# Performance work log

Measured on AMD Instinct MI355X. Metric: run time of the kernel, lower is better.

Reference implementation:

```python
import jax, jax.numpy as jnp
import numpy as np

NUM_HEADS = 4
EMBED_DIM = 256
HEAD_DIM = EMBED_DIM // NUM_HEADS
B, N = 4, 4096


def setup_inputs() -> dict:
    key = jax.random.key(0)
    kq, kk, kv, kw = jax.random.split(key, 4)
    q = jax.random.normal(kq, (B, N, EMBED_DIM), dtype=jnp.float32)
    k = jax.random.normal(kk, (B, N, EMBED_DIM), dtype=jnp.float32)
    v = jax.random.normal(kv, (B, N, EMBED_DIM), dtype=jnp.float32)
    W_out = jax.random.normal(kw, (EMBED_DIM, EMBED_DIM), dtype=jnp.float32) * (1.0 / np.sqrt(EMBED_DIM))
    b_out = jnp.zeros((EMBED_DIM,), dtype=jnp.float32)
    return {"q": q, "k": k, "v": v, "W_out": W_out, "b_out": b_out}


def reference(q, k, v, W_out, b_out):
    b, n, _ = q.shape
    # [b, n, e] -> [b, h, n, d]
    qh = q.reshape(b, n, NUM_HEADS, HEAD_DIM).transpose(0, 2, 1, 3)
    kh = k.reshape(b, n, NUM_HEADS, HEAD_DIM).transpose(0, 2, 1, 3)
    vh = v.reshape(b, n, NUM_HEADS, HEAD_DIM).transpose(0, 2, 1, 3)
    scale = 1.0 / jnp.sqrt(jnp.asarray(HEAD_DIM, dtype=qh.dtype))
    # full [b, h, n, n] score matrix, as in the original module
    attn = jnp.einsum('bhqd,bhkd->bhqk', qh, kh) * scale
    attn = jax.nn.softmax(attn, axis=-1)
    out = jnp.einsum('bhqk,bhkd->bhqd', attn, vh)
    out = out.transpose(0, 2, 1, 3).reshape(b, n, EMBED_DIM)
    # nn.Linear: x @ W.T + b
    return out @ W_out.T + b_out
```

## Files before the change

kernel.cpp:

```cpp
#include <hip/hip_runtime.h>
#include <hip/hip_bf16.h>

#define B_ 4
#define H_ 4
#define N_ 4096
#define D_ 64
#define E_ 256
#define KVB 64
#define QBLK 128
#define NT (N_ / KVB)

typedef short short8 __attribute__((ext_vector_type(8)));
typedef float f32x4 __attribute__((ext_vector_type(4)));
typedef float f32x16 __attribute__((ext_vector_type(16)));

__device__ __forceinline__ ushort f2bf(float f) {
  union { float f; unsigned u; } a; a.f = f;
  unsigned r = a.u + 0x7fffu + ((a.u >> 16) & 1u);
  return (ushort)(r >> 16);
}

__device__ __forceinline__ uint4 pack8(float a0, float a1, float a2, float a3,
                                       float a4, float a5, float a6, float a7) {
  uint4 u;
  u.x = (unsigned)f2bf(a0) | ((unsigned)f2bf(a1) << 16);
  u.y = (unsigned)f2bf(a2) | ((unsigned)f2bf(a3) << 16);
  u.z = (unsigned)f2bf(a4) | ((unsigned)f2bf(a5) << 16);
  u.w = (unsigned)f2bf(a6) | ((unsigned)f2bf(a7) << 16);
  return u;
}

__device__ __forceinline__ unsigned cvt_pk_bf16(float lo, float hi) {
  unsigned r;
  asm("v_cvt_pk_bf16_f32 %0, %1, %2" : "=v"(r) : "v"(lo), "v"(hi));
  return r;
}

__device__ __forceinline__ void permlane32_swap(unsigned &a, unsigned &b) {
  asm volatile("v_permlane32_swap_b32 %0, %1" : "+v"(a), "+v"(b));
}

__global__ void cast_w_kernel(const float* __restrict__ W, ushort* __restrict__ Wb) {
  int i = blockIdx.x * blockDim.x + threadIdx.x;
  float4 x = ((const float4*)W)[i];
  ushort4 o;
  o.x = f2bf(x.x); o.y = f2bf(x.y); o.z = f2bf(x.z); o.w = f2bf(x.w);
  ((ushort4*)Wb)[i] = o;
}

__global__ void prep_kv(const float* __restrict__ k, const float* __restrict__ v,
                        ushort* __restrict__ Kb, ushort* __restrict__ Vtb) {
  __shared__ float kt[64][65];
  __shared__ float vt[64][65];
  const int gid = blockIdx.x;
  const int bh = gid >> 6, t = gid & 63;
  const int b = bh >> 2, h = bh & 3;
  const int tid = threadIdx.x;
  const int rr = tid >> 4, cc = (tid & 15) * 4;
  const float* kg = k + ((size_t)b * N_ + t * 64) * E_ + h * 64;
  const float* vg = v + ((size_t)b * N_ + t * 64) * E_ + h * 64;
  ushort* ko = Kb + (size_t)gid * 4096;
  ushort* vo = Vtb + (size_t)gid * 4096;

  for (int it = 0; it < 4; ++it) {
    int r = rr + it * 16;
    float4 kx = *(const float4*)(kg + (size_t)r * E_ + cc);
    float4 vx = *(const float4*)(vg + (size_t)r * E_ + cc);
    kt[r][cc] = kx.x; kt[r][cc + 1] = kx.y; kt[r][cc + 2] = kx.z; kt[r][cc + 3] = kx.w;
    vt[r][cc] = vx.x; vt[r][cc + 1] = vx.y; vt[r][cc + 2] = vx.z; vt[r][cc + 3] = vx.w;
  }
  __syncthreads();

  for (int j = 0; j < 2; ++j) {
    int u = j * 256 + tid;
    int frag = u >> 6, l = u & 63;
    int a = (frag >> 2) * 32 + (l & 31);
    int c0 = (frag & 3) * 16 + ((l >> 5) & 1) * 8;
    *(uint4*)(ko + u * 8) = pack8(kt[a][c0], kt[a][c0 + 1], kt[a][c0 + 2], kt[a][c0 + 3],
                                  kt[a][c0 + 4], kt[a][c0 + 5], kt[a][c0 + 6], kt[a][c0 + 7]);
    *(uint4*)(vo + u * 8) = pack8(vt[c0][a], vt[c0 + 1][a], vt[c0 + 2][a], vt[c0 + 3][a],
                                  vt[c0 + 4][a], vt[c0 + 5][a], vt[c0 + 6][a], vt[c0 + 7][a]);
  }
}

__launch_bounds__(256, 2)
__global__ void attn_kernel(const float* __restrict__ q,
                            const ushort* __restrict__ Kb,
                            const ushort* __restrict__ Vtb,
                            ushort* __restrict__ X) {
  __shared__ __attribute__((aligned(16))) ushort SM[2][2][4096];
  __shared__ float Lb[2][2][32];
  __shared__ float Lb2[2][2][32];

  const int bid = blockIdx.x;
  const int swz = (bid & 7) * 64 + (bid >> 3);
  const int bh = swz >> 5;
  const int qt = swz & 31;
  const int b = bh >> 2, h = bh & 3;
  const int tid = threadIdx.x;
  const int wid = tid >> 6;
  const int wq = wid & 1;
  const int kh = wid >> 1;
  const int lane = tid & 63;
  const int ln = lane & 31;
  const int hi = lane >> 5;

  const char* Kg = (const char*)Kb + (size_t)bh * NT * 8192;
  const char* Vg = (const char*)Vtb + (size_t)bh * NT * 8192;

  const float SC = 0.125f * 1.44269504f;
  const int qrow0 = qt * QBLK + wq * 64;
  short8 qf[2][4];
#pragma unroll
  for (int qg = 0; qg < 2; ++qg) {
    const float* Qg = q + ((size_t)b * N_ + qrow0 + qg * 32 + ln) * E_ + h * D_;
#pragma unroll
    for (int ks = 0; ks < 4; ++ks) {
      const float* p = Qg + ks * 16 + hi * 8;
      float4 x0 = *(const float4*)(p);
      float4 x1 = *(const float4*)(p + 4);
      short8 f;
      f[0] = (short)f2bf(x0.x * SC); f[1] = (short)f2bf(x0.y * SC);
      f[2] = (short)f2bf(x0.z * SC); f[3] = (short)f2bf(x0.w * SC);
      f[4] = (short)f2bf(x1.x * SC); f[5] = (short)f2bf(x1.y * SC);
      f[6] = (short)f2bf(x1.z * SC); f[7] = (short)f2bf(x1.w * SC);
      qf[qg][ks] = f;
    }
  }

  f32x16 O00 = (f32x16)0.0f, O01 = (f32x16)0.0f;
  f32x16 O10 = (f32x16)0.0f, O11 = (f32x16)0.0f;
  float lsum0 = 0.f, lsum1 = 0.f;

  {
    uint4 a0 = *(const uint4*)(Kg + tid * 16);
    uint4 a1 = *(const uint4*)(Kg + 4096 + tid * 16);
    uint4 a2 = *(const uint4*)(Vg + tid * 16);
    uint4 a3 = *(const uint4*)(Vg + 4096 + tid * 16);
    *(uint4*)((char*)&SM[0][0][0] + tid * 16) = a0;
    *(uint4*)((char*)&SM[0][0][0] + 4096 + tid * 16) = a1;
    *(uint4*)((char*)&SM[0][1][0] + tid * 16) = a2;
    *(uint4*)((char*)&SM[0][1][0] + 4096 + tid * 16) = a3;
  }
  __syncthreads();
  int cur = 0;

  for (int t = 0; t < NT; ++t) {
    const bool pfn = (t + 1 < NT);
    uint4 rk0, rk1, rv0, rv1;
    if (pfn) {
      const char* kg = Kg + (size_t)(t + 1) * 8192;
      const char* vg = Vg + (size_t)(t + 1) * 8192;
      rk0 = *(const uint4*)(kg + tid * 16);
      rk1 = *(const uint4*)(kg + 4096 + tid * 16);
      rv0 = *(const uint4*)(vg + tid * 16);
      rv1 = *(const uint4*)(vg + 4096 + tid * 16);
    }

    const char* Kl = (const char*)&SM[cur][0][0];
    const char* Vl = (const char*)&SM[cur][1][0];

    short8 kf[4];
#pragma unroll
    for (int ks = 0; ks < 4; ++ks)
      kf[ks] = *(short8*)(Kl + (kh * 4 + ks) * 1024 + lane * 16);

    f32x16 S0 = (f32x16)0.0f, S1 = (f32x16)0.0f;
    __builtin_amdgcn_s_setprio(1);
#pragma unroll
    for (int ks = 0; ks < 4; ++ks) {
      S0 = __builtin_amdgcn_mfma_f32_32x32x16_bf16(kf[ks], qf[0][ks], S0, 0, 0, 0);
      S1 = __builtin_amdgcn_mfma_f32_32x32x16_bf16(kf[ks], qf[1][ks], S1, 0, 0, 0);
    }
    __builtin_amdgcn_s_setprio(0);

    short8 vf[2][2];
#pragma unroll
    for (int db = 0; db < 2; ++db)
#pragma unroll
      for (int s = 0; s < 2; ++s)
        vf[db][s] = *(short8*)(Vl + (db * 4 + kh * 2 + s) * 1024 + lane * 16);

    float p0[16], p1[16];
#pragma unroll
    for (int i = 0; i < 16; ++i) {
      p0[i] = __builtin_amdgcn_exp2f(S0[i]);
      p1[i] = __builtin_amdgcn_exp2f(S1[i]);
    }
    {
      float s1[8];
#pragma unroll
      for (int i = 0; i < 8; ++i) s1[i] = p0[2 * i] + p0[2 * i + 1];
#pragma unroll
      for (int i = 0; i < 4; ++i) s1[i] = s1[2 * i] + s1[2 * i + 1];
      lsum0 += (s1[0] + s1[1]) + (s1[2] + s1[3]);
#pragma unroll
      for (int i = 0; i < 8; ++i) s1[i] = p1[2 * i] + p1[2 * i + 1];
#pragma unroll
      for (int i = 0; i < 4; ++i) s1[i] = s1[2 * i] + s1[2 * i + 1];
      lsum1 += (s1[0] + s1[1]) + (s1[2] + s1[3]);
    }

    short8 pa0[2], pa1[2];
#pragma unroll
    for (int s = 0; s < 2; ++s) {
      int base = s * 8;
      {
        unsigned w0 = cvt_pk_bf16(p0[base + 0], p0[base + 1]);
        unsigned w2 = cvt_pk_bf16(p0[base + 4], p0[base + 5]);
        permlane32_swap(w0, w2);
        unsigned w1 = cvt_pk_bf16(p0[base + 2], p0[base + 3]);
        unsigned w3 = cvt_pk_bf16(p0[base + 6], p0[base + 7]);
        permlane32_swap(w1, w3);
        uint4 u; u.x = w0; u.y = w1; u.z = w2; u.w = w3;
        union { uint4 u4; short8 s8; } cv; cv.u4 = u;
        pa0[s] = cv.s8;
      }
      {
        unsigned w0 = cvt_pk_bf16(p1[base + 0], p1[base + 1]);
        unsigned w2 = cvt_pk_bf16(p1[base + 4], p1[base + 5]);
        permlane32_swap(w0, w2);
        unsigned w1 = cvt_pk_bf16(p1[base + 2], p1[base + 3]);
        unsigned w3 = cvt_pk_bf16(p1[base + 6], p1[base + 7]);
        permlane32_swap(w1, w3);
        uint4 u; u.x = w0; u.y = w1; u.z = w2; u.w = w3;
        union { uint4 u4; short8 s8; } cv; cv.u4 = u;
        pa1[s] = cv.s8;
      }
    }

    if (pfn) {
      *(uint4*)((char*)&SM[cur ^ 1][0][0] + tid * 16) = rk0;
      *(uint4*)((char*)&SM[cur ^ 1][0][0] + 4096 + tid * 16) = rk1;
      *(uint4*)((char*)&SM[cur ^ 1][1][0] + tid * 16) = rv0;
      *(uint4*)((char*)&SM[cur ^ 1][1][0] + 4096 + tid * 16) = rv1;
    }

    __builtin_amdgcn_s_setprio(1);
#pragma unroll
    for (int s = 0; s < 2; ++s) {
      O00 = __builtin_amdgcn_mfma_f32_32x32x16_bf16(pa0[s], vf[0][s], O00, 0, 0, 0);
      O01 = __builtin_amdgcn_mfma_f32_32x32x16_bf16(pa0[s], vf[1][s], O01, 0, 0, 0);
      O10 = __builtin_amdgcn_mfma_f32_32x32x16_bf16(pa1[s], vf[0][s], O10, 0, 0, 0);
      O11 = __builtin_amdgcn_mfma_f32_32x32x16_bf16(pa1[s], vf[1][s], O11, 0, 0, 0);
    }
    __builtin_amdgcn_s_setprio(0);

    __syncthreads();
    cur ^= 1;
  }

  float l0 = lsum0 + __shfl_xor(lsum0, 32);
  float l1 = lsum1 + __shfl_xor(lsum1, 32);
  float* Ox = (float*)&SM[0][0][0];
  if (kh) {
    if (lane < 32) { Lb[wq][0][ln] = l0; Lb[wq][1][ln] = l1; }
#pragma unroll
    for (int r2 = 0; r2 < 16; ++r2) {
      Ox[wq * 4096 + 0 * 2048 + 0 * 1024 + r2 * 64 + lane] = O00[r2];
      Ox[wq * 4096 + 0 * 2048 + 1 * 1024 + r2 * 64 + lane] = O01[r2];
      Ox[wq * 4096 + 1 * 2048 + 0 * 1024 + r2 * 64 + lane] = O10[r2];
      Ox[wq * 4096 + 1 * 2048 + 1 * 1024 + r2 * 64 + lane] = O11[r2];
    }
  }
  __syncthreads();
  if (!kh) {
    float lt0 = l0 + Lb[wq][0][ln];
    float lt1 = l1 + Lb[wq][1][ln];
    if (lane < 32) { Lb2[wq][0][ln] = lt0; Lb2[wq][1][ln] = lt1; }
    asm volatile("" ::: "memory");
#pragma unroll
    for (int r2 = 0; r2 < 16; ++r2) {
      O00[r2] += Ox[wq * 4096 + 0 * 2048 + 0 * 1024 + r2 * 64 + lane];
      O01[r2] += Ox[wq * 4096 + 0 * 2048 + 1 * 1024 + r2 * 64 + lane];
      O10[r2] += Ox[wq * 4096 + 1 * 2048 + 0 * 1024 + r2 * 64 + lane];
      O11[r2] += Ox[wq * 4096 + 1 * 2048 + 1 * 1024 + r2 * 64 + lane];
    }
    ushort* Xp = X + ((size_t)b * N_) * E_ + h * D_;
#pragma unroll
    for (int r2 = 0; r2 < 16; ++r2) {
      int crow = (r2 & 3) + 8 * (r2 >> 2) + 4 * hi;
      float i0 = 1.0f / Lb2[wq][0][crow];
      float i1 = 1.0f / Lb2[wq][1][crow];
      int q0 = qrow0 + crow;
      int q1 = qrow0 + 32 + crow;
      Xp[(size_t)q0 * E_ + ln]      = f2bf(O00[r2] * i0);
      Xp[(size_t)q0 * E_ + 32 + ln] = f2bf(O01[r2] * i0);
      Xp[(size_t)q1 * E_ + ln]      = f2bf(O10[r2] * i1);
      Xp[(size_t)q1 * E_ + 32 + ln] = f2bf(O11[r2] * i1);
    }
  }
}

__launch_bounds__(256, 2)
__global__ void proj_kernel(const ushort* __restrict__ X, const ushort* __restrict__ Wb,
                            const float* __restrict__ bias, float* __restrict__ out) {
  const int m0   = blockIdx.x * 64;
  const int tid  = threadIdx.x;
  const int wid  = tid >> 6;
  const int lane = tid & 63;
  const int g    = lane >> 4;
  const int lr   = lane & 15;
  const int n0   = wid * 64;

  f32x4 acc[4][4];
  for (int mb = 0; mb < 4; ++mb)
    for (int nb = 0; nb < 4; ++nb)
      acc[mb][nb] = (f32x4){0.f, 0.f, 0.f, 0.f};

  for (int k0 = 0; k0 < E_; k0 += 32) {
    short8 af[4], bfr[4];
    for (int mb = 0; mb < 4; ++mb)
      af[mb] = *(const short8*)(X + (size_t)(m0 + mb * 16 + lr) * E_ + k0 + g * 8);
    for (int nb = 0; nb < 4; ++nb)
      bfr[nb] = *(const short8*)(Wb + (size_t)(n0 + nb * 16 + lr) * E_ + k0 + g * 8);
    for (int mb = 0; mb < 4; ++mb)
      for (int nb = 0; nb < 4; ++nb)
        acc[mb][nb] = __builtin_amdgcn_mfma_f32_16x16x32_bf16(af[mb], bfr[nb], acc[mb][nb], 0, 0, 0);
  }

  for (int nb = 0; nb < 4; ++nb) {
    float bv = bias[n0 + nb * 16 + lr];
    for (int mb = 0; mb < 4; ++mb)
      for (int r = 0; r < 4; ++r)
        out[(size_t)(m0 + mb * 16 + g * 4 + r) * E_ + n0 + nb * 16 + lr] = acc[mb][nb][r] + bv;
  }
}

extern "C" void kernel_launch(void* const* d_in, const int* in_sizes, int n_in,
                              void* d_out, int out_size, void* d_ws, size_t ws_size,
                              hipStream_t stream) {
  const float* q    = (const float*)d_in[0];
  const float* k    = (const float*)d_in[1];
  const float* v    = (const float*)d_in[2];
  const float* W    = (const float*)d_in[3];
  const float* bias = (const float*)d_in[4];

  char* ws = (char*)d_ws;
  ushort* X   = (ushort*)ws;
  ushort* Wb  = (ushort*)(ws + 8388608);
  ushort* Kb  = (ushort*)(ws + 8388608 + 131072);
  ushort* Vtb = (ushort*)(ws + 8388608 + 131072 + 8388608);

  cast_w_kernel<<<64, 256, 0, stream>>>(W, Wb);
  prep_kv<<<B_ * H_ * NT, 256, 0, stream>>>(k, v, Kb, Vtb);
  attn_kernel<<<B_ * H_ * (N_ / QBLK), 256, 0, stream>>>(q, Kb, Vtb, X);
  proj_kernel<<<(B_ * N_) / 64, 256, 0, stream>>>(X, Wb, bias, (float*)d_out);
}
```

Measured before the change: 108.9 us.

## Process two KV tiles per loop iteration with doubled shared-memory stages

The attention main loop now handles two 64-key tiles per iteration. The shared buffers are doubled to hold a pair of K/V tiles, and the prefetch of the next pair is issued after both QK^T MFMA groups. This halves the number of block-wide barriers and lets the second tile's score MFMAs overlap with the first tile's softmax and PV work. In exchange it doubles LDS usage to 64KB and needs more registers for the extra score accumulators and 8 prefetch registers, which may reduce occupancy under the 2-blocks-per-CU launch bound.

```diff
diff --git a/kernel.cpp b/kernel.cpp
--- a/kernel.cpp
+++ b/kernel.cpp
@@ -9,6 +9,7 @@
 #define KVB 64
 #define QBLK 128
 #define NT (N_ / KVB)
+#define NR (NT / 2)
 
 typedef short short8 __attribute__((ext_vector_type(8)));
 typedef float f32x4 __attribute__((ext_vector_type(4)));
@@ -88,7 +89,7 @@
                             const ushort* __restrict__ Kb,
                             const ushort* __restrict__ Vtb,
                             ushort* __restrict__ X) {
-  __shared__ __attribute__((aligned(16))) ushort SM[2][2][4096];
+  __shared__ __attribute__((aligned(16))) ushort SM[2][2][2][4096];
   __shared__ float Lb[2][2][32];
   __shared__ float Lb2[2][2][32];
 
@@ -133,118 +134,211 @@
   float lsum0 = 0.f, lsum1 = 0.f;
 
   {
-    uint4 a0 = *(const uint4*)(Kg + tid * 16);
-    uint4 a1 = *(const uint4*)(Kg + 4096 + tid * 16);
-    uint4 a2 = *(const uint4*)(Vg + tid * 16);
-    uint4 a3 = *(const uint4*)(Vg + 4096 + tid * 16);
-    *(uint4*)((char*)&SM[0][0][0] + tid * 16) = a0;
-    *(uint4*)((char*)&SM[0][0][0] + 4096 + tid * 16) = a1;
-    *(uint4*)((char*)&SM[0][1][0] + tid * 16) = a2;
-    *(uint4*)((char*)&SM[0][1][0] + 4096 + tid * 16) = a3;
+#pragma unroll
+    for (int c = 0; c < 2; ++c) {
+      uint4 a0 = *(const uint4*)(Kg + (size_t)c * 8192 + tid * 16);
+      uint4 a1 = *(const uint4*)(Kg + (size_t)c * 8192 + 4096 + tid * 16);
+      uint4 a2 = *(const uint4*)(Vg + (size_t)c * 8192 + tid * 16);
+      uint4 a3 = *(const uint4*)(Vg + (size_t)c * 8192 + 4096 + tid * 16);
+      *(uint4*)((char*)&SM[0][c][0][0] + tid * 16) = a0;
+      *(uint4*)((char*)&SM[0][c][0][0] + 4096 + tid * 16) = a1;
+      *(uint4*)((char*)&SM[0][c][1][0] + tid * 16) = a2;
+      *(uint4*)((char*)&SM[0][c][1][0] + 4096 + tid * 16) = a3;
+    }
   }
   __syncthreads();
   int cur = 0;
 
-  for (int t = 0; t < NT; ++t) {
-    const bool pfn = (t + 1 < NT);
-    uint4 rk0, rk1, rv0, rv1;
+  for (int r = 0; r < NR; ++r) {
+    const bool pfn = (r + 1 < NR);
+
+    const char* KlA = (const char*)&SM[cur][0][0][0];
+    const char* VlA = (const char*)&SM[cur][0][1][0];
+    const char* KlB = (const char*)&SM[cur][1][0][0];
+    const char* VlB = (const char*)&SM[cur][1][1][0];
+
+    short8 kfA[4];
+#pragma unroll
+    for (int ks = 0; ks < 4; ++ks)
+      kfA[ks] = *(short8*)(KlA + (kh * 4 + ks) * 1024 + lane * 16);
+    f32x16 SA0 = (f32x16)0.0f, SA1 = (f32x16)0.0f;
+    __builtin_amdgcn_s_setprio(1);
+#pragma unroll
+    for (int ks = 0; ks < 4; ++ks) {
+      SA0 = __builtin_amdgcn_mfma_f32_32x32x16_bf16(kfA[ks], qf[0][ks], SA0, 0, 0, 0);
+      SA1 = __builtin_amdgcn_mfma_f32_32x32x16_bf16(kfA[ks], qf[1][ks], SA1, 0, 0, 0);
+    }
+    __builtin_amdgcn_s_setprio(0);
+
+    short8 kfB[4];
+#pragma unroll
+    for (int ks = 0; ks < 4; ++ks)
+      kfB[ks] = *(short8*)(KlB + (kh * 4 + ks) * 1024 + lane * 16);
+    f32x16 SB0 = (f32x16)0.0f, SB1 = (f32x16)0.0f;
+    __builtin_amdgcn_s_setprio(1);
+#pragma unroll
+    for (int ks = 0; ks < 4; ++ks) {
+      SB0 = __builtin_amdgcn_mfma_f32_32x32x16_bf16(kfB[ks], qf[0][ks], SB0, 0, 0, 0);
+      SB1 = __builtin_amdgcn_mfma_f32_32x32x16_bf16(kfB[ks], qf[1][ks], SB1, 0, 0, 0);
+    }
+    __builtin_amdgcn_s_setprio(0);
+
+    uint4 st[8];
     if (pfn) {
-      const char* kg = Kg + (size_t)(t + 1) * 8192;
-      const char* vg = Vg + (size_t)(t + 1) * 8192;
-      rk0 = *(const uint4*)(kg + tid * 16);
-      rk1 = *(const uint4*)(kg + 4096 + tid * 16);
-      rv0 = *(const uint4*)(vg + tid * 16);
-      rv1 = *(const uint4*)(vg + 4096 + tid * 16);
-    }
-
-    const char* Kl = (const char*)&SM[cur][0][0];
-    const char* Vl = (const char*)&SM[cur][1][0];
-
-    short8 kf[4];
-#pragma unroll
-    for (int ks = 0; ks < 4; ++ks)
-      kf[ks] = *(short8*)(Kl + (kh * 4 + ks) * 1024 + lane * 16);
-
-    f32x16 S0 = (f32x16)0.0f, S1 = (f32x16)0.0f;
-    __builtin_amdgcn_s_setprio(1);
-#pragma unroll
-    for (int ks = 0; ks < 4; ++ks) {
-      S0 = __builtin_amdgcn_mfma_f32_32x32x16_bf16(kf[ks], qf[0][ks], S0, 0, 0, 0);
-      S1 = __builtin_amdgcn_mfma_f32_32x32x16_bf16(kf[ks], qf[1][ks], S1, 0, 0, 0);
-    }
-    __builtin_amdgcn_s_setprio(0);
-
-    short8 vf[2][2];
-#pragma unroll
-    for (int db = 0; db < 2; ++db)
-#pragma unroll
-      for (int s = 0; s < 2; ++s)
-        vf[db][s] = *(short8*)(Vl + (db * 4 + kh * 2 + s) * 1024 + lane * 16);
-
-    float p0[16], p1[16];
-#pragma unroll
-    for (int i = 0; i < 16; ++i) {
-      p0[i] = __builtin_amdgcn_exp2f(S0[i]);
-      p1[i] = __builtin_amdgcn_exp2f(S1[i]);
-    }
+      const char* kg = Kg + (size_t)(2 * r + 2) * 8192;
+      const char* vg = Vg + (size_t)(2 * r + 2) * 8192;
+#pragma unroll
+      for (int c = 0; c < 2; ++c) {
+        st[c * 4 + 0] = *(const uint4*)(kg + (size_t)c * 8192 + tid * 16);
+        st[c * 4 + 1] = *(const uint4*)(kg + (size_t)c * 8192 + 4096 + tid * 16);
+        st[c * 4 + 2] = *(const uint4*)(vg + (size_t)c * 8192 + tid * 16);
+        st[c * 4 + 3] = *(const uint4*)(vg + (size_t)c * 8192 + 4096 + tid * 16);
+      }
+    }
+
     {
-      float s1[8];
-#pragma unroll
-      for (int i = 0; i < 8; ++i) s1[i] = p0[2 * i] + p0[2 * i + 1];
-#pragma unroll
-      for (int i = 0; i < 4; ++i) s1[i] = s1[2 * i] + s1[2 * i + 1];
-      lsum0 += (s1[0] + s1[1]) + (s1[2] + s1[3]);
-#pragma unroll
-      for (int i = 0; i < 8; ++i) s1[i] = p1[2 * i] + p1[2 * i + 1];
-#pragma unroll
-      for (int i = 0; i < 4; ++i) s1[i] = s1[2 * i] + s1[2 * i + 1];
-      lsum1 += (s1[0] + s1[1]) + (s1[2] + s1[3]);
-    }
-
-    short8 pa0[2], pa1[2];
-#pragma unroll
-    for (int s = 0; s < 2; ++s) {
-      int base = s * 8;
+      short8 vf[2][2];
+#pragma unroll
+      for (int db = 0; db < 2; ++db)
+#pragma unroll
+        for (int s = 0; s < 2; ++s)
+          vf[db][s] = *(short8*)(VlA + (db * 4 + kh * 2 + s) * 1024 + lane * 16);
+
+      float p0[16], p1[16];
+#pragma unroll
+      for (int i = 0; i < 16; ++i) {
+        p0[i] = __builtin_amdgcn_exp2f(SA0[i]);
+        p1[i] = __builtin_amdgcn_exp2f(SA1[i]);
+      }
       {
-        unsigned w0 = cvt_pk_bf16(p0[base + 0], p0[base + 1]);
-        unsigned w2 = cvt_pk_bf16(p0[base + 4], p0[base + 5]);
-        permlane32_swap(w0, w2);
-        unsigned w1 = cvt_pk_bf16(p0[base + 2], p0[base + 3]);
-        unsigned w3 = cvt_pk_bf16(p0[base + 6], p0[base + 7]);
-        permlane32_swap(w1, w3);
-        uint4 u; u.x = w0; u.y = w1; u.z = w2; u.w = w3;
-        union { uint4 u4; short8 s8; } cv; cv.u4 = u;
-        pa0[s] = cv.s8;
+        float s1[8];
+#pragma unroll
+        for (int i = 0; i < 8; ++i) s1[i] = p0[2 * i] + p0[2 * i + 1];
+#pragma unroll
+        for (int i = 0; i < 4; ++i) s1[i] = s1[2 * i] + s1[2 * i + 1];
+        lsum0 += (s1[0] + s1[1]) + (s1[2] + s1[3]);
+#pragma unroll
+        for (int i = 0; i < 8; ++i) s1[i] = p1[2 * i] + p1[2 * i + 1];
+#pragma unroll
+        for (int i = 0; i < 4; ++i) s1[i] = s1[2 * i] + s1[2 * i + 1];
+        lsum1 += (s1[0] + s1[1]) + (s1[2] + s1[3]);
+      }
+
+      short8 pa0[2], pa1[2];
+#pragma unroll
+      for (int s = 0; s < 2; ++s) {
+        int base = s * 8;
+        {
+          unsigned w0 = cvt_pk_bf16(p0[base + 0], p0[base + 1]);
+          unsigned w2 = cvt_pk_bf16(p0[base + 4], p0[base + 5]);
+          permlane32_swap(w0, w2);
+          unsigned w1 = cvt_pk_bf16(p0[base + 2], p0[base + 3]);
+          unsigned w3 = cvt_pk_bf16(p0[base + 6], p0[base + 7]);
+          permlane32_swap(w1, w3);
+          uint4 u; u.x = w0; u.y = w1; u.z = w2; u.w = w3;
+          union { uint4 u4; short8 s8; } cv; cv.u4 = u;
+          pa0[s] = cv.s8;
+        }
+        {
+          unsigned w0 = cvt_pk_bf16(p1[base + 0], p1[base + 1]);
+          unsigned w2 = cvt_pk_bf16(p1[base + 4], p1[base + 5]);
+          permlane32_swap(w0, w2);
+          unsigned w1 = cvt_pk_bf16(p1[base + 2], p1[base + 3]);
+          unsigned w3 = cvt_pk_bf16(p1[base + 6], p1[base + 7]);
+          permlane32_swap(w1, w3);
+          uint4 u; u.x = w0; u.y = w1; u.z = w2; u.w = w3;
+          union { uint4 u4; short8 s8; } cv; cv.u4 = u;
+          pa1[s] = cv.s8;
+        }
+      }
+
+      __builtin_amdgcn_s_setprio(1);
+#pragma unroll
+      for (int s = 0; s < 2; ++s) {
+        O00 = __builtin_amdgcn_mfma_f32_32x32x16_bf16(pa0[s], vf[0][s], O00, 0, 0, 0);
+        O01 = __builtin_amdgcn_mfma_f32_32x32x16_bf16(pa0[s], vf[1][s], O01, 0, 0, 0);
+        O10 = __builtin_amdgcn_mfma_f32_32x32x16_bf16(pa1[s], vf[0][s], O10, 0, 0, 0);
+        O11 = __builtin_amdgcn_mfma_f32_32x32x16_bf16(pa1[s], vf[1][s], O11, 0, 0, 0);
+      }
+      __builtin_amdgcn_s_setprio(0);
+    }
+
+    {
+      short8 vf[2][2];
+#pragma unroll
+      for (int db = 0; db < 2; ++db)
+#pragma unroll
+        for (int s = 0; s < 2; ++s)
+          vf[db][s] = *(short8*)(VlB + (db * 4 + kh * 2 + s) * 1024 + lane * 16);
+
+      float p0[16], p1[16];
+#pragma unroll
+      for (int i = 0; i < 16; ++i) {
+        p0[i] = __builtin_amdgcn_exp2f(SB0[i]);
+        p1[i] = __builtin_amdgcn_exp2f(SB1[i]);
       }
       {
-        unsigned w0 = cvt_pk_bf16(p1[base + 0], p1[base + 1]);
-        unsigned w2 = cvt_pk_bf16(p1[base + 4], p1[base + 5]);
-        permlane32_swap(w0, w2);
-        unsigned w1 = cvt_pk_bf16(p1[base + 2], p1[base + 3]);
-        unsigned w3 = cvt_pk_bf16(p1[base + 6], p1[base + 7]);
-        permlane32_swap(w1, w3);
-        uint4 u; u.x = w0; u.y = w1; u.z = w2; u.w = w3;
-        union { uint4 u4; short8 s8; } cv; cv.u4 = u;
-        pa1[s] = cv.s8;
-      }
+        float s1[8];
+#pragma unroll
+        for (int i = 0; i < 8; ++i) s1[i] = p0[2 * i] + p0[2 * i + 1];
+#pragma unroll
+        for (int i = 0; i < 4; ++i) s1[i] = s1[2 * i] + s1[2 * i + 1];
+        lsum0 += (s1[0] + s1[1]) + (s1[2] + s1[3]);
+#pragma unroll
+        for (int i = 0; i < 8; ++i) s1[i] = p1[2 * i] + p1[2 * i + 1];
+#pragma unroll
+        for (int i = 0; i < 4; ++i) s1[i] = s1[2 * i] + s1[2 * i + 1];
+        lsum1 += (s1[0] + s1[1]) + (s1[2] + s1[3]);
+      }
+
+      short8 pa0[2], pa1[2];
+#pragma unroll
+      for (int s = 0; s < 2; ++s) {
+        int base = s * 8;
+        {
+          unsigned w0 = cvt_pk_bf16(p0[base + 0], p0[base + 1]);
+          unsigned w2 = cvt_pk_bf16(p0[base + 4], p0[base + 5]);
+          permlane32_swap(w0, w2);
+          unsigned w1 = cvt_pk_bf16(p0[base + 2], p0[base + 3]);
+          unsigned w3 = cvt_pk_bf16(p0[base + 6], p0[base + 7]);
+          permlane32_swap(w1, w3);
+          uint4 u; u.x = w0; u.y = w1; u.z = w2; u.w = w3;
+          union { uint4 u4; short8 s8; } cv; cv.u4 = u;
+          pa0[s] = cv.s8;
+        }
+        {
+          unsigned w0 = cvt_pk_bf16(p1[base + 0], p1[base + 1]);
+          unsigned w2 = cvt_pk_bf16(p1[base + 4], p1[base + 5]);
+          permlane32_swap(w0, w2);
+          unsigned w1 = cvt_pk_bf16(p1[base + 2], p1[base + 3]);
+          unsigned w3 = cvt_pk_bf16(p1[base + 6], p1[base + 7]);
+          permlane32_swap(w1, w3);
+          uint4 u; u.x = w0; u.y = w1; u.z = w2; u.w = w3;
+          union { uint4 u4; short8 s8; } cv; cv.u4 = u;
+          pa1[s] = cv.s8;
+        }
+      }
+
+      __builtin_amdgcn_s_setprio(1);
+#pragma unroll
+      for (int s = 0; s < 2; ++s) {
+        O00 = __builtin_amdgcn_mfma_f32_32x32x16_bf16(pa0[s], vf[0][s], O00, 0, 0, 0);
+        O01 = __builtin_amdgcn_mfma_f32_32x32x16_bf16(pa0[s], vf[1][s], O01, 0, 0, 0);
+        O10 = __builtin_amdgcn_mfma_f32_32x32x16_bf16(pa1[s], vf[0][s], O10, 0, 0, 0);
+        O11 = __builtin_amdgcn_mfma_f32_32x32x16_bf16(pa1[s], vf[1][s], O11, 0, 0, 0);
+      }
+      __builtin_amdgcn_s_setprio(0);
     }
 
     if (pfn) {
-      *(uint4*)((char*)&SM[cur ^ 1][0][0] + tid * 16) = rk0;
-      *(uint4*)((char*)&SM[cur ^ 1][0][0] + 4096 + tid * 16) = rk1;
-      *(uint4*)((char*)&SM[cur ^ 1][1][0] + tid * 16) = rv0;
-      *(uint4*)((char*)&SM[cur ^ 1][1][0] + 4096 + tid * 16) = rv1;
-    }
-
-    __builtin_amdgcn_s_setprio(1);
-#pragma unroll
-    for (int s = 0; s < 2; ++s) {
-      O00 = __builtin_amdgcn_mfma_f32_32x32x16_bf16(pa0[s], vf[0][s], O00, 0, 0, 0);
-      O01 = __builtin_amdgcn_mfma_f32_32x32x16_bf16(pa0[s], vf[1][s], O01, 0, 0, 0);
-      O10 = __builtin_amdgcn_mfma_f32_32x32x16_bf16(pa1[s], vf[0][s], O10, 0, 0, 0);
-      O11 = __builtin_amdgcn_mfma_f32_32x32x16_bf16(pa1[s], vf[1][s], O11, 0, 0, 0);
-    }
-    __builtin_amdgcn_s_setprio(0);
+#pragma unroll
+      for (int c = 0; c < 2; ++c) {
+        *(uint4*)((char*)&SM[cur ^ 1][c][0][0] + tid * 16) = st[c * 4 + 0];
+        *(uint4*)((char*)&SM[cur ^ 1][c][0][0] + 4096 + tid * 16) = st[c * 4 + 1];
+        *(uint4*)((char*)&SM[cur ^ 1][c][1][0] + tid * 16) = st[c * 4 + 2];
+        *(uint4*)((char*)&SM[cur ^ 1][c][1][0] + 4096 + tid * 16) = st[c * 4 + 3];
+      }
+    }
 
     __syncthreads();
     cur ^= 1;
@@ -252,7 +346,7 @@
 
   float l0 = lsum0 + __shfl_xor(lsum0, 32);
   float l1 = lsum1 + __shfl_xor(lsum1, 32);
-  float* Ox = (float*)&SM[0][0][0];
+  float* Ox = (float*)&SM[0][0][0][0];
   if (kh) {
     if (lane < 32) { Lb[wq][0][ln] = l0; Lb[wq][1][ln] = l1; }
 #pragma unroll
```

Result: slower. 112.2 us (+3.0%).
